# Optimization experiments

Measured on AMD Instinct MI355X. Metric: run time of the kernel, lower is better.

The kernel has to match this reference:

```python
import jax, jax.numpy as jnp
import numpy as np

EPS = 1e-07


def setup_inputs() -> dict:
    key = jax.random.key(0)
    ks = jax.random.split(key, 5)
    B, Cin, Cout, H, W, K, S = 8, 512, 512, 64, 64, 3, 512
    return {
        "x": jax.random.normal(ks[0], (B, Cin, H, W), dtype=jnp.float32),
        "style": jax.random.normal(ks[1], (B, S), dtype=jnp.float32),
        "weight": jax.random.normal(ks[2], (1, Cout, Cin, K, K), dtype=jnp.float32),
        "mod_w": jax.random.normal(ks[3], (Cin, S), dtype=jnp.float32) * (1.0 / np.sqrt(S)),
        "mod_b": jax.random.normal(ks[4], (Cin,), dtype=jnp.float32) * 0.01,
    }


def reference(x, style, weight, mod_w, mod_b):
    B, Cin, H, W = x.shape
    Cout, K = weight.shape[1], weight.shape[3]
    scale = 1.0 / np.sqrt(Cin * K * K)
    # modulation: plain linear (EqualLinear.forward never applies self.scale)
    s = (style @ mod_w.T + mod_b).reshape(B, 1, Cin, 1, 1)
    w = scale * weight * s  # [B, Cout, Cin, K, K]
    demod = jax.lax.rsqrt(jnp.sum(w * w, axis=(2, 3, 4), keepdims=True) + EPS)
    # NOTE: source divides by rsqrt (i.e. multiplies by sqrt) -- kept faithful
    w = w / demod
    w = w.reshape(B * Cout, Cin, K, K)
    xr = x.reshape(1, B * Cin, H, W)
    pad = (K - 1) // 2
    out = jax.lax.conv_general_dilated(
        xr, w,
        window_strides=(1, 1),
        padding=((pad, pad), (pad, pad)),
        dimension_numbers=("NCHW", "OIHW", "NCHW"),
        feature_group_count=B,
    )
    return out.reshape(B, Cout, H, W)
```

## Files before the change

kernel.cpp:

```cpp
#include <hip/hip_runtime.h>
#include <hip/hip_bf16.h>
#include <stdint.h>
#include <math.h>

#define EPSV 1e-7f
#define B_   8
#define CIN  512
#define COUT 512
#define HH   64
#define WW   64
#define SS   512
#define HP   66
#define WP   66
#define NP   (HH*WW)

typedef __attribute__((ext_vector_type(8))) short bf16x8;
typedef __attribute__((ext_vector_type(4))) float f32x4;

__global__ __launch_bounds__(256) void k_style(const float* __restrict__ style,
                                               const float* __restrict__ mod_w,
                                               const float* __restrict__ mod_b,
                                               float* __restrict__ s_out) {
    int tid = threadIdx.x;
    int id = blockIdx.x * 64 + (tid >> 2);
    int b = id >> 9, ci = id & 511, q = tid & 3;
    const float4* st = (const float4*)(style + (size_t)b * SS);
    const float4* mw = (const float4*)(mod_w + (size_t)ci * SS);
    float acc = 0.f;
    #pragma unroll
    for (int j = 0; j < 32; ++j) {
        float4 s4 = st[q * 32 + j];
        float4 w4 = mw[q * 32 + j];
        acc += s4.x * w4.x + s4.y * w4.y + s4.z * w4.z + s4.w * w4.w;
    }
    acc += __shfl_xor(acc, 1);
    acc += __shfl_xor(acc, 2);
    if (q == 0) s_out[id] = acc + mod_b[ci];
}

__global__ __launch_bounds__(256) void k_wmod(const float* __restrict__ weight,
                                              const float* __restrict__ s_in,
                                              __hip_bfloat16* __restrict__ wmod) {
    const int co  = blockIdx.x;
    const int tid = threadIdx.x;
    const int lane = tid & 63, wid = tid >> 6;
    const float scale = 0.014731391274719739f;
    float wv0[9], wv1[9];
    float wsq0 = 0.f, wsq1 = 0.f;
    {
        const float* wp0 = weight + ((size_t)co * CIN + tid) * 9;
        const float* wp1 = weight + ((size_t)co * CIN + tid + 256) * 9;
        #pragma unroll
        for (int t = 0; t < 9; ++t) { wv0[t] = wp0[t]; wsq0 += wv0[t] * wv0[t]; }
        #pragma unroll
        for (int t = 0; t < 9; ++t) { wv1[t] = wp1[t]; wsq1 += wv1[t] * wv1[t]; }
    }
    float sv0[8], sv1[8], sqb[8];
    #pragma unroll
    for (int b = 0; b < 8; ++b) {
        sv0[b] = s_in[b * CIN + tid] * scale;
        sv1[b] = s_in[b * CIN + tid + 256] * scale;
        sqb[b] = sv0[b] * sv0[b] * wsq0 + sv1[b] * sv1[b] * wsq1;
    }
    #pragma unroll
    for (int b = 0; b < 8; ++b) {
        float v = sqb[b];
        #pragma unroll
        for (int off = 32; off > 0; off >>= 1) v += __shfl_xor(v, off);
        sqb[b] = v;
    }
    __shared__ float red[4][8];
    if (lane == 0) {
        #pragma unroll
        for (int b = 0; b < 8; ++b) red[wid][b] = sqb[b];
    }
    __syncthreads();
    float dfac[8];
    #pragma unroll
    for (int b = 0; b < 8; ++b)
        dfac[b] = sqrtf(red[0][b] + red[1][b] + red[2][b] + red[3][b] + EPSV);
    #pragma unroll
    for (int b = 0; b < 8; ++b) {
        #pragma unroll
        for (int t = 0; t < 9; ++t) {
            size_t rowbase = ((size_t)((b * 9 + t) * COUT) + co) * CIN;
            wmod[rowbase + tid]       = __float2bfloat16(wv0[t] * sv0[b] * dfac[b]);
            wmod[rowbase + tid + 256] = __float2bfloat16(wv1[t] * sv1[b] * dfac[b]);
        }
    }
}

__global__ __launch_bounds__(256) void k_xpad(const float* __restrict__ x,
                                              __hip_bfloat16* __restrict__ xpad) {
    const int b = blockIdx.x >> 6;
    const int h = blockIdx.x & 63;
    const int tid = threadIdx.x;
    __shared__ float tile[64][65];
    for (int ci0 = 0; ci0 < CIN; ci0 += 64) {
        #pragma unroll
        for (int it = 0; it < 4; ++it) {
            int idx = it * 256 + tid;
            int w4 = idx & 15, cil = idx >> 4;
            float4 v = *(const float4*)&x[(((size_t)b * CIN + ci0 + cil) * HH + h) * WW + 4 * w4];
            tile[cil][4 * w4 + 0] = v.x; tile[cil][4 * w4 + 1] = v.y;
            tile[cil][4 * w4 + 2] = v.z; tile[cil][4 * w4 + 3] = v.w;
        }
        __syncthreads();
        #pragma unroll
        for (int it = 0; it < 4; ++it) {
            int idx = it * 256 + tid;
            int c4 = idx & 15, w = idx >> 4;
            __hip_bfloat16 t0 = __float2bfloat16(tile[4 * c4 + 0][w]);
            __hip_bfloat16 t1 = __float2bfloat16(tile[4 * c4 + 1][w]);
            __hip_bfloat16 t2 = __float2bfloat16(tile[4 * c4 + 2][w]);
            __hip_bfloat16 t3 = __float2bfloat16(tile[4 * c4 + 3][w]);
            ushort4 pk = make_ushort4(*(unsigned short*)&t0, *(unsigned short*)&t1,
                                      *(unsigned short*)&t2, *(unsigned short*)&t3);
            *(ushort4*)&xpad[(((size_t)b * HP + h + 1) * WP + (w + 1)) * CIN + ci0 + 4 * c4] = pk;
        }
        __syncthreads();
    }
    const size_t base = (size_t)b * HP * WP * CIN;
    const ushort4 z4 = make_ushort4(0, 0, 0, 0);
    {
        int wp = (tid < 128) ? 0 : 65;
        int e  = (tid & 127) * 4;
        *(ushort4*)&xpad[base + ((size_t)(h + 1) * WP + wp) * CIN + e] = z4;
    }
    if (h == 0 || h == 63) {
        int hp = (h == 0) ? 0 : 65;
        for (int i = tid; i < (HP * CIN) / 4; i += 256)
            *(ushort4*)&xpad[base + (size_t)hp * WP * CIN + (size_t)i * 4] = z4;
    }
}


#define MM(A,B,C) __builtin_amdgcn_mfma_f32_16x16x32_bf16(A,B,C,0,0,0)

#define GLDS(GP, LOFF) __builtin_amdgcn_global_load_lds( \
    (const __attribute__((address_space(1))) void*)(GP), \
    (__attribute__((address_space(3))) void*)(smem + (LOFF)), 16, 0, 0)

#define LDA(SB, M) (*(const bf16x8*)(aLds + ((SB)*16384 + (M)*1024)))
#define LDB(SB, N) (*(const bf16x8*)(bLds + ((SB)*16384 + (N)*1024)))

#define STAGE_A(KT, SB) { const int t3_ = (KT) >> 4, ci3_ = ((KT) & 15) * 32;   \
    const size_t aB_ = (size_t)(bb * 9 + t3_) * (COUT * CIN) + ci3_;            \
    GLDS(wmod + aB_ + gA0, (SB) * 16384 + ldsd);                                \
    GLDS(wmod + aB_ + gA1, (SB) * 16384 + 8192 + ldsd); }

#define STAGE_B(KT, SB) { const int t3_ = (KT) >> 4, ci3_ = ((KT) & 15) * 32;   \
    const int bO_ = ((t3_ / 3) * WP + (t3_ % 3)) * CIN + ci3_;                  \
    GLDS(xpad + bO_ + gB0, 65536 + (SB) * 16384 + ldsd);                        \
    GLDS(xpad + bO_ + gB1, 65536 + (SB) * 16384 + 8192 + ldsd); }

#define BARRIER asm volatile("s_barrier" ::: "memory")
#define VM8 asm volatile("s_waitcnt vmcnt(8)" ::: "memory");
#define VM4 asm volatile("s_waitcnt vmcnt(4)" ::: "memory");
#define VM0 asm volatile("s_waitcnt vmcnt(0)" ::: "memory");
#define VMNONE

#define CCOL(N, BV) acc[0][N]=MM(ca0,BV,acc[0][N]); acc[1][N]=MM(ca1,BV,acc[1][N]); \
                    acc[2][N]=MM(ca2,BV,acc[2][N]); acc[3][N]=MM(ca3,BV,acc[3][N]);
#define XCOL(N, BV) acc[4][N]=MM(x4_,BV,acc[4][N]); acc[5][N]=MM(x5_,BV,acc[5][N]); \
                    acc[6][N]=MM(x6_,BV,acc[6][N]); acc[7][N]=MM(x7_,BV,acc[7][N]);

#define KTILE3(KK, SB, DOSTAGE, WAITER, DONEXT) {                               \
    cb2 = LDB(SB, 2); cb3 = LDB(SB, 3);                                         \
    bf16x8 x4_ = LDA(SB,4), x5_ = LDA(SB,5), x6_ = LDA(SB,6), x7_ = LDA(SB,7);  \
    if (DOSTAGE) { STAGE_A((KK)+3, ((SB)+3)&3); STAGE_B((KK)+3, ((SB)+3)&3); }  \
    __builtin_amdgcn_s_setprio(1);                                              \
    CCOL(0, cb0) CCOL(1, cb1) CCOL(2, cb2) CCOL(3, cb3)                         \
    __builtin_amdgcn_s_setprio(0);                                              \
    __builtin_amdgcn_sched_barrier(0);                                          \
    WAITER                                                                      \
    BARRIER;                                                                    \
    __builtin_amdgcn_sched_barrier(0);                                          \
    if (DONEXT) { const int nsb_ = ((SB)+1)&3;                                  \
        ca0 = LDA(nsb_,0); ca1 = LDA(nsb_,1);                                   \
        ca2 = LDA(nsb_,2); ca3 = LDA(nsb_,3);                                   \
        nb0_ = LDB(nsb_,0); nb1_ = LDB(nsb_,1);                                 \
    }                                                                           \
    __builtin_amdgcn_s_setprio(1);                                              \
    XCOL(0, cb0) XCOL(1, cb1) XCOL(2, cb2) XCOL(3, cb3)                         \
    __builtin_amdgcn_s_setprio(0);                                              \
    cb0 = nb0_; cb1 = nb1_;                                                     \
}

__global__ __launch_bounds__(512, 2) void k_conv(const __hip_bfloat16* __restrict__ wmod,
                                                 const __hip_bfloat16* __restrict__ xpad,
                                                 float* __restrict__ out) {
    __shared__ __align__(16) char smem[131072];

    const int tid  = threadIdx.x;
    const int lane = tid & 63;
    const int wid  = tid >> 6;
    const int wr   = wid >> 2;
    const int wc   = wid & 3;
    const int frow = lane & 15;
    const int fk   = lane >> 4;

    const int bid = blockIdx.x;
    const int bb  = bid & 7;
    const int pt  = (bid >> 3) & 15;
    const int ct  = bid >> 7;
    const int co0 = ct * 256;
    const int p0  = pt * 256;

    const int xr = (fk ^ ((frow >> 1) & 3)) * 16;
    const char* aLds = smem + (wr * 8192 + frow * 64 + xr);
    const char* bLds = smem + 65536 + (wc * 4096 + frow * 64 + xr);

    const int ldsd = wid * 1024 + lane * 16;
    const int srow = wid * 16 + (lane >> 2);
    const int cg   = ((lane & 3) ^ ((lane >> 3) & 3)) * 8;
    const int gA0  = (co0 + srow) * CIN + cg;
    const int gA1  = (co0 + 128 + srow) * CIN + cg;
    const int pp0  = p0 + srow;
    const int pp1  = p0 + 128 + srow;
    const int gB0  = ((bb * HP + (pp0 >> 6)) * WP + (pp0 & 63)) * CIN + cg;
    const int gB1  = ((bb * HP + (pp1 >> 6)) * WP + (pp1 & 63)) * CIN + cg;

    f32x4 acc[8][4];
    #pragma unroll
    for (int m = 0; m < 8; ++m)
        #pragma unroll
        for (int n = 0; n < 4; ++n)
            acc[m][n] = (f32x4){0.f, 0.f, 0.f, 0.f};

    bf16x8 ca0, ca1, ca2, ca3, cb0, cb1, cb2, cb3, nb0_, nb1_;

    STAGE_A(0, 0) STAGE_B(0, 0)
    STAGE_A(1, 1) STAGE_B(1, 1)
    STAGE_A(2, 2) STAGE_B(2, 2)
    VM8;
    BARRIER;
    ca0 = LDA(0, 0); ca1 = LDA(0, 1); ca2 = LDA(0, 2); ca3 = LDA(0, 3);
    cb0 = LDB(0, 0); cb1 = LDB(0, 1);

    for (int k4 = 0; k4 < 140; k4 += 4) {
        KTILE3(k4 + 0, 0, 1, VM8, 1)
        KTILE3(k4 + 1, 1, 1, VM8, 1)
        KTILE3(k4 + 2, 2, 1, VM8, 1)
        KTILE3(k4 + 3, 3, 1, VM8, 1)
    }
    KTILE3(140, 0, 1, VM8, 1)
    KTILE3(141, 1, 0, VM4, 1)
    KTILE3(142, 2, 0, VM0, 1)
    KTILE3(143, 3, 0, VMNONE, 0)

    #pragma unroll
    for (int m = 0; m < 8; ++m) {
        int co = co0 + wr * 128 + m * 16 + fk * 4;
        #pragma unroll
        for (int n = 0; n < 4; ++n) {
            int p = p0 + wc * 64 + n * 16 + frow;
            #pragma unroll
            for (int j = 0; j < 4; ++j)
                out[((size_t)(bb * COUT + co + j)) * NP + p] = acc[m][n][j];
        }
    }
}

extern "C" void kernel_launch(void* const* d_in, const int* in_sizes, int n_in,
                              void* d_out, int out_size, void* d_ws, size_t ws_size,
                              hipStream_t stream) {
    const float* x      = (const float*)d_in[0];
    const float* style  = (const float*)d_in[1];
    const float* weight = (const float*)d_in[2];
    const float* mod_w  = (const float*)d_in[3];
    const float* mod_b  = (const float*)d_in[4];
    float* out = (float*)d_out;

    char* ws = (char*)d_ws;
    const size_t S_OFF    = 0;
    const size_t WMOD_OFF = 16384;
    const size_t XPAD_OFF = WMOD_OFF + (size_t)B_ * 9 * COUT * CIN * 2;

    float*          s_buf = (float*)(ws + S_OFF);
    __hip_bfloat16* wmod  = (__hip_bfloat16*)(ws + WMOD_OFF);
    __hip_bfloat16* xpad  = (__hip_bfloat16*)(ws + XPAD_OFF);

    k_style<<<64, 256, 0, stream>>>(style, mod_w, mod_b, s_buf);
    k_xpad<<<B_ * HH, 256, 0, stream>>>(x, xpad);
    k_wmod<<<512, 256, 0, stream>>>(weight, s_buf, wmod);

    k_conv<<<256, 512, 0, stream>>>(wmod, xpad, out);
}
```

Before: 160.5 us.

## Fold modulation into input and demod into epilogue; switch conv to 32x32 MFMA

The per-batch modulated weight tensor (8x9x512x512 bf16) is no longer built. The style scale is applied to the input during padding/bf16 conversion, and the demodulation factor is applied to the conv output in the epilogue. This shares one bf16 weight copy across batches and cuts weight-prep traffic. Separately, the conv inner loop moves from 16x16x32 to 32x32x16 bf16 MFMA with a new LDS read layout and fewer A/B fragment loads per tile. Rounding changes because the scale is now rounded into the bf16 input rather than the weights, and the new fragment indexing must match the existing swizzled LDS staging.

```diff
diff --git a/kernel.cpp b/kernel.cpp
--- a/kernel.cpp
+++ b/kernel.cpp
@@ -14,13 +14,16 @@
 #define WP   66
 #define NP   (HH*WW)
 
-typedef __attribute__((ext_vector_type(8))) short bf16x8;
-typedef __attribute__((ext_vector_type(4))) float f32x4;
-
-__global__ __launch_bounds__(256) void k_style(const float* __restrict__ style,
-                                               const float* __restrict__ mod_w,
-                                               const float* __restrict__ mod_b,
-                                               float* __restrict__ s_out) {
+typedef __attribute__((ext_vector_type(8)))  short bf16x8;
+typedef __attribute__((ext_vector_type(4)))  float f32x4;
+typedef __attribute__((ext_vector_type(16))) float f32x16;
+
+#define MODSCALE 0.014731391274719739f
+
+__global__ __launch_bounds__(256) void k_mod(const float* __restrict__ style,
+                                             const float* __restrict__ mod_w,
+                                             const float* __restrict__ mod_b,
+                                             float* __restrict__ m_out) {
     int tid = threadIdx.x;
     int id = blockIdx.x * 64 + (tid >> 2);
     int b = id >> 9, ci = id & 511, q = tid & 3;
@@ -35,62 +38,51 @@
     }
     acc += __shfl_xor(acc, 1);
     acc += __shfl_xor(acc, 2);
-    if (q == 0) s_out[id] = acc + mod_b[ci];
-}
-
-__global__ __launch_bounds__(256) void k_wmod(const float* __restrict__ weight,
-                                              const float* __restrict__ s_in,
-                                              __hip_bfloat16* __restrict__ wmod) {
-    const int co  = blockIdx.x;
+    if (q == 0) m_out[id] = MODSCALE * (acc + mod_b[ci]);
+}
+
+__global__ __launch_bounds__(256) void k_wprep(const float* __restrict__ weight,
+                                               __hip_bfloat16* __restrict__ wt,
+                                               float* __restrict__ wsq) {
+    const int co = blockIdx.x;
     const int tid = threadIdx.x;
-    const int lane = tid & 63, wid = tid >> 6;
-    const float scale = 0.014731391274719739f;
-    float wv0[9], wv1[9];
-    float wsq0 = 0.f, wsq1 = 0.f;
-    {
-        const float* wp0 = weight + ((size_t)co * CIN + tid) * 9;
-        const float* wp1 = weight + ((size_t)co * CIN + tid + 256) * 9;
-        #pragma unroll
-        for (int t = 0; t < 9; ++t) { wv0[t] = wp0[t]; wsq0 += wv0[t] * wv0[t]; }
-        #pragma unroll
-        for (int t = 0; t < 9; ++t) { wv1[t] = wp1[t]; wsq1 += wv1[t] * wv1[t]; }
-    }
-    float sv0[8], sv1[8], sqb[8];
-    #pragma unroll
-    for (int b = 0; b < 8; ++b) {
-        sv0[b] = s_in[b * CIN + tid] * scale;
-        sv1[b] = s_in[b * CIN + tid + 256] * scale;
-        sqb[b] = sv0[b] * sv0[b] * wsq0 + sv1[b] * sv1[b] * wsq1;
-    }
-    #pragma unroll
-    for (int b = 0; b < 8; ++b) {
-        float v = sqb[b];
-        #pragma unroll
-        for (int off = 32; off > 0; off >>= 1) v += __shfl_xor(v, off);
-        sqb[b] = v;
-    }
-    __shared__ float red[4][8];
-    if (lane == 0) {
-        #pragma unroll
-        for (int b = 0; b < 8; ++b) red[wid][b] = sqb[b];
-    }
-    __syncthreads();
-    float dfac[8];
-    #pragma unroll
-    for (int b = 0; b < 8; ++b)
-        dfac[b] = sqrtf(red[0][b] + red[1][b] + red[2][b] + red[3][b] + EPSV);
-    #pragma unroll
-    for (int b = 0; b < 8; ++b) {
-        #pragma unroll
-        for (int t = 0; t < 9; ++t) {
-            size_t rowbase = ((size_t)((b * 9 + t) * COUT) + co) * CIN;
-            wmod[rowbase + tid]       = __float2bfloat16(wv0[t] * sv0[b] * dfac[b]);
-            wmod[rowbase + tid + 256] = __float2bfloat16(wv1[t] * sv1[b] * dfac[b]);
-        }
-    }
+    #pragma unroll
+    for (int j = 0; j < 2; ++j) {
+        int ci = tid + j * 256;
+        const float* wp = weight + ((size_t)co * CIN + ci) * 9;
+        float w[9], sq = 0.f;
+        #pragma unroll
+        for (int t = 0; t < 9; ++t) { w[t] = wp[t]; sq += w[t] * w[t]; }
+        #pragma unroll
+        for (int t = 0; t < 9; ++t)
+            wt[(size_t)t * COUT * CIN + (size_t)co * CIN + ci] = __float2bfloat16(w[t]);
+        wsq[co * CIN + ci] = sq;
+    }
+}
+
+__global__ __launch_bounds__(256) void k_dfac(const float* __restrict__ wsq,
+                                              const float* __restrict__ m_buf,
+                                              float* __restrict__ dfac) {
+    int tid = threadIdx.x;
+    int id = blockIdx.x * 64 + (tid >> 2);
+    int b = id >> 9, co = id & 511, q = tid & 3;
+    const float4* wq = (const float4*)(wsq + (size_t)co * CIN);
+    const float4* mb = (const float4*)(m_buf + (size_t)b * CIN);
+    float acc = 0.f;
+    #pragma unroll
+    for (int j = 0; j < 32; ++j) {
+        float4 w4 = wq[q * 32 + j];
+        float4 m4 = mb[q * 32 + j];
+        acc += w4.x * m4.x * m4.x + w4.y * m4.y * m4.y
+             + w4.z * m4.z * m4.z + w4.w * m4.w * m4.w;
+    }
+    acc += __shfl_xor(acc, 1);
+    acc += __shfl_xor(acc, 2);
+    if (q == 0) dfac[id] = sqrtf(acc + EPSV);
 }
 
 __global__ __launch_bounds__(256) void k_xpad(const float* __restrict__ x,
+                                              const float* __restrict__ m_buf,
                                               __hip_bfloat16* __restrict__ xpad) {
     const int b = blockIdx.x >> 6;
     const int h = blockIdx.x & 63;
@@ -110,10 +102,11 @@
         for (int it = 0; it < 4; ++it) {
             int idx = it * 256 + tid;
             int c4 = idx & 15, w = idx >> 4;
-            __hip_bfloat16 t0 = __float2bfloat16(tile[4 * c4 + 0][w]);
-            __hip_bfloat16 t1 = __float2bfloat16(tile[4 * c4 + 1][w]);
-            __hip_bfloat16 t2 = __float2bfloat16(tile[4 * c4 + 2][w]);
-            __hip_bfloat16 t3 = __float2bfloat16(tile[4 * c4 + 3][w]);
+            float4 mv = *(const float4*)&m_buf[b * CIN + ci0 + 4 * c4];
+            __hip_bfloat16 t0 = __float2bfloat16(tile[4 * c4 + 0][w] * mv.x);
+            __hip_bfloat16 t1 = __float2bfloat16(tile[4 * c4 + 1][w] * mv.y);
+            __hip_bfloat16 t2 = __float2bfloat16(tile[4 * c4 + 2][w] * mv.z);
+            __hip_bfloat16 t3 = __float2bfloat16(tile[4 * c4 + 3][w] * mv.w);
             ushort4 pk = make_ushort4(*(unsigned short*)&t0, *(unsigned short*)&t1,
                                       *(unsigned short*)&t2, *(unsigned short*)&t3);
             *(ushort4*)&xpad[(((size_t)b * HP + h + 1) * WP + (w + 1)) * CIN + ci0 + 4 * c4] = pk;
@@ -135,19 +128,19 @@
 }
 
 
-#define MM(A,B,C) __builtin_amdgcn_mfma_f32_16x16x32_bf16(A,B,C,0,0,0)
+#define MM32(A,B,C) __builtin_amdgcn_mfma_f32_32x32x16_bf16(A,B,C,0,0,0)
 
 #define GLDS(GP, LOFF) __builtin_amdgcn_global_load_lds( \
     (const __attribute__((address_space(1))) void*)(GP), \
     (__attribute__((address_space(3))) void*)(smem + (LOFF)), 16, 0, 0)
 
-#define LDA(SB, M) (*(const bf16x8*)(aLds + ((SB)*16384 + (M)*1024)))
-#define LDB(SB, N) (*(const bf16x8*)(bLds + ((SB)*16384 + (N)*1024)))
+#define LDA32(SB, M, XR) (*(const bf16x8*)(aBase + ((SB)*16384 + (M)*2048 + (XR))))
+#define LDB32(SB, N, XR) (*(const bf16x8*)(bBase + ((SB)*16384 + (N)*2048 + (XR))))
 
 #define STAGE_A(KT, SB) { const int t3_ = (KT) >> 4, ci3_ = ((KT) & 15) * 32;   \
-    const size_t aB_ = (size_t)(bb * 9 + t3_) * (COUT * CIN) + ci3_;            \
-    GLDS(wmod + aB_ + gA0, (SB) * 16384 + ldsd);                                \
-    GLDS(wmod + aB_ + gA1, (SB) * 16384 + 8192 + ldsd); }
+    const size_t aB_ = (size_t)t3_ * (COUT * CIN) + ci3_;                       \
+    GLDS(wt + aB_ + gA0, (SB) * 16384 + ldsd);                                  \
+    GLDS(wt + aB_ + gA1, (SB) * 16384 + 8192 + ldsd); }
 
 #define STAGE_B(KT, SB) { const int t3_ = (KT) >> 4, ci3_ = ((KT) & 15) * 32;   \
     const int bO_ = ((t3_ / 3) * WP + (t3_ % 3)) * CIN + ci3_;                  \
@@ -160,35 +153,36 @@
 #define VM0 asm volatile("s_waitcnt vmcnt(0)" ::: "memory");
 #define VMNONE
 
-#define CCOL(N, BV) acc[0][N]=MM(ca0,BV,acc[0][N]); acc[1][N]=MM(ca1,BV,acc[1][N]); \
-                    acc[2][N]=MM(ca2,BV,acc[2][N]); acc[3][N]=MM(ca3,BV,acc[3][N]);
-#define XCOL(N, BV) acc[4][N]=MM(x4_,BV,acc[4][N]); acc[5][N]=MM(x5_,BV,acc[5][N]); \
-                    acc[6][N]=MM(x6_,BV,acc[6][N]); acc[7][N]=MM(x7_,BV,acc[7][N]);
-
-#define KTILE3(KK, SB, DOSTAGE, WAITER, DONEXT) {                               \
-    cb2 = LDB(SB, 2); cb3 = LDB(SB, 3);                                         \
-    bf16x8 x4_ = LDA(SB,4), x5_ = LDA(SB,5), x6_ = LDA(SB,6), x7_ = LDA(SB,7);  \
+#define CL(A0,A1,A2,A3,B0,B1) \
+    acc[0][0]=MM32(A0,B0,acc[0][0]); acc[1][0]=MM32(A1,B0,acc[1][0]); \
+    acc[2][0]=MM32(A2,B0,acc[2][0]); acc[3][0]=MM32(A3,B0,acc[3][0]); \
+    acc[0][1]=MM32(A0,B1,acc[0][1]); acc[1][1]=MM32(A1,B1,acc[1][1]); \
+    acc[2][1]=MM32(A2,B1,acc[2][1]); acc[3][1]=MM32(A3,B1,acc[3][1]);
+
+#define KTILE32(KK, SB, DOSTAGE, WAITER, DONEXT) {                              \
+    bf16x8 a10=LDA32(SB,0,xr1), a11=LDA32(SB,1,xr1),                            \
+           a12=LDA32(SB,2,xr1), a13=LDA32(SB,3,xr1);                            \
+    bf16x8 b10=LDB32(SB,0,xr1), b11=LDB32(SB,1,xr1);                            \
     if (DOSTAGE) { STAGE_A((KK)+3, ((SB)+3)&3); STAGE_B((KK)+3, ((SB)+3)&3); }  \
     __builtin_amdgcn_s_setprio(1);                                              \
-    CCOL(0, cb0) CCOL(1, cb1) CCOL(2, cb2) CCOL(3, cb3)                         \
+    CL(a00,a01,a02,a03,b00,b01)                                                 \
     __builtin_amdgcn_s_setprio(0);                                              \
     __builtin_amdgcn_sched_barrier(0);                                          \
     WAITER                                                                      \
     BARRIER;                                                                    \
     __builtin_amdgcn_sched_barrier(0);                                          \
     if (DONEXT) { const int nsb_ = ((SB)+1)&3;                                  \
-        ca0 = LDA(nsb_,0); ca1 = LDA(nsb_,1);                                   \
-        ca2 = LDA(nsb_,2); ca3 = LDA(nsb_,3);                                   \
-        nb0_ = LDB(nsb_,0); nb1_ = LDB(nsb_,1);                                 \
-    }                                                                           \
+        a00=LDA32(nsb_,0,xr0); a01=LDA32(nsb_,1,xr0);                           \
+        a02=LDA32(nsb_,2,xr0); a03=LDA32(nsb_,3,xr0);                           \
+        b00=LDB32(nsb_,0,xr0); b01=LDB32(nsb_,1,xr0); }                         \
     __builtin_amdgcn_s_setprio(1);                                              \
-    XCOL(0, cb0) XCOL(1, cb1) XCOL(2, cb2) XCOL(3, cb3)                         \
+    CL(a10,a11,a12,a13,b10,b11)                                                 \
     __builtin_amdgcn_s_setprio(0);                                              \
-    cb0 = nb0_; cb1 = nb1_;                                                     \
-}
-
-__global__ __launch_bounds__(512, 2) void k_conv(const __hip_bfloat16* __restrict__ wmod,
+}
+
+__global__ __launch_bounds__(512, 2) void k_conv(const __hip_bfloat16* __restrict__ wt,
                                                  const __hip_bfloat16* __restrict__ xpad,
+                                                 const float* __restrict__ dfac,
                                                  float* __restrict__ out) {
     __shared__ __align__(16) char smem[131072];
 
@@ -197,8 +191,8 @@
     const int wid  = tid >> 6;
     const int wr   = wid >> 2;
     const int wc   = wid & 3;
-    const int frow = lane & 15;
-    const int fk   = lane >> 4;
+    const int l31  = lane & 31;
+    const int hi   = lane >> 5;
 
     const int bid = blockIdx.x;
     const int bb  = bid & 7;
@@ -207,9 +201,11 @@
     const int co0 = ct * 256;
     const int p0  = pt * 256;
 
-    const int xr = (fk ^ ((frow >> 1) & 3)) * 16;
-    const char* aLds = smem + (wr * 8192 + frow * 64 + xr);
-    const char* bLds = smem + 65536 + (wc * 4096 + frow * 64 + xr);
+    const int swz = (l31 >> 1) & 3;
+    const int xr0 = ((0 + hi) ^ swz) * 16;
+    const int xr1 = ((2 + hi) ^ swz) * 16;
+    const char* aBase = smem + ((wr * 128 + l31) * 64);
+    const char* bBase = smem + 65536 + ((wc * 64 + l31) * 64);
 
     const int ldsd = wid * 1024 + lane * 16;
     const int srow = wid * 16 + (lane >> 2);
@@ -221,43 +217,46 @@
     const int gB0  = ((bb * HP + (pp0 >> 6)) * WP + (pp0 & 63)) * CIN + cg;
     const int gB1  = ((bb * HP + (pp1 >> 6)) * WP + (pp1 & 63)) * CIN + cg;
 
-    f32x4 acc[8][4];
-    #pragma unroll
-    for (int m = 0; m < 8; ++m)
-        #pragma unroll
-        for (int n = 0; n < 4; ++n)
-            acc[m][n] = (f32x4){0.f, 0.f, 0.f, 0.f};
-
-    bf16x8 ca0, ca1, ca2, ca3, cb0, cb1, cb2, cb3, nb0_, nb1_;
+    f32x16 acc[4][2];
+    #pragma unroll
+    for (int m = 0; m < 4; ++m)
+        #pragma unroll
+        for (int n = 0; n < 2; ++n)
+            acc[m][n] = (f32x16)(0.f);
+
+    bf16x8 a00, a01, a02, a03, b00, b01;
 
     STAGE_A(0, 0) STAGE_B(0, 0)
     STAGE_A(1, 1) STAGE_B(1, 1)
     STAGE_A(2, 2) STAGE_B(2, 2)
     VM8;
     BARRIER;
-    ca0 = LDA(0, 0); ca1 = LDA(0, 1); ca2 = LDA(0, 2); ca3 = LDA(0, 3);
-    cb0 = LDB(0, 0); cb1 = LDB(0, 1);
+    a00 = LDA32(0,0,xr0); a01 = LDA32(0,1,xr0); a02 = LDA32(0,2,xr0); a03 = LDA32(0,3,xr0);
+    b00 = LDB32(0,0,xr0); b01 = LDB32(0,1,xr0);
 
     for (int k4 = 0; k4 < 140; k4 += 4) {
-        KTILE3(k4 + 0, 0, 1, VM8, 1)
-        KTILE3(k4 + 1, 1, 1, VM8, 1)
-        KTILE3(k4 + 2, 2, 1, VM8, 1)
-        KTILE3(k4 + 3, 3, 1, VM8, 1)
-    }
-    KTILE3(140, 0, 1, VM8, 1)
-    KTILE3(141, 1, 0, VM4, 1)
-    KTILE3(142, 2, 0, VM0, 1)
-    KTILE3(143, 3, 0, VMNONE, 0)
-
-    #pragma unroll
-    for (int m = 0; m < 8; ++m) {
-        int co = co0 + wr * 128 + m * 16 + fk * 4;
-        #pragma unroll
-        for (int n = 0; n < 4; ++n) {
-            int p = p0 + wc * 64 + n * 16 + frow;
+        KTILE32(k4 + 0, 0, 1, VM8, 1)
+        KTILE32(k4 + 1, 1, 1, VM8, 1)
+        KTILE32(k4 + 2, 2, 1, VM8, 1)
+        KTILE32(k4 + 3, 3, 1, VM8, 1)
+    }
+    KTILE32(140, 0, 1, VM8, 1)
+    KTILE32(141, 1, 0, VM4, 1)
+    KTILE32(142, 2, 0, VM0, 1)
+    KTILE32(143, 3, 0, VMNONE, 0)
+
+    const float* dfb = dfac + bb * COUT + co0 + wr * 128;
+    #pragma unroll
+    for (int m = 0; m < 4; ++m) {
+        #pragma unroll
+        for (int n = 0; n < 2; ++n) {
+            int p = p0 + wc * 64 + n * 32 + l31;
             #pragma unroll
-            for (int j = 0; j < 4; ++j)
-                out[((size_t)(bb * COUT + co + j)) * NP + p] = acc[m][n][j];
+            for (int r = 0; r < 16; ++r) {
+                int row = m * 32 + (r & 3) + 8 * (r >> 2) + 4 * hi;
+                out[((size_t)(bb * COUT + co0 + wr * 128 + row)) * NP + p] =
+                    acc[m][n][r] * dfb[row];
+            }
         }
     }
 }
@@ -273,17 +272,22 @@
     float* out = (float*)d_out;
 
     char* ws = (char*)d_ws;
-    const size_t S_OFF    = 0;
-    const size_t WMOD_OFF = 16384;
-    const size_t XPAD_OFF = WMOD_OFF + (size_t)B_ * 9 * COUT * CIN * 2;
-
-    float*          s_buf = (float*)(ws + S_OFF);
-    __hip_bfloat16* wmod  = (__hip_bfloat16*)(ws + WMOD_OFF);
+    const size_t M_OFF    = 0;
+    const size_t WSQ_OFF  = 16384;
+    const size_t DFAC_OFF = WSQ_OFF + (size_t)COUT * CIN * 4;
+    const size_t WT_OFF   = DFAC_OFF + 16384;
+    const size_t XPAD_OFF = WT_OFF + (size_t)9 * COUT * CIN * 2;
+
+    float*          m_buf = (float*)(ws + M_OFF);
+    float*          wsq   = (float*)(ws + WSQ_OFF);
+    float*          dfac  = (float*)(ws + DFAC_OFF);
+    __hip_bfloat16* wt    = (__hip_bfloat16*)(ws + WT_OFF);
     __hip_bfloat16* xpad  = (__hip_bfloat16*)(ws + XPAD_OFF);
 
-    k_style<<<64, 256, 0, stream>>>(style, mod_w, mod_b, s_buf);
-    k_xpad<<<B_ * HH, 256, 0, stream>>>(x, xpad);
-    k_wmod<<<512, 256, 0, stream>>>(weight, s_buf, wmod);
-
-    k_conv<<<256, 512, 0, stream>>>(wmod, xpad, out);
-}
+    k_mod<<<64, 256, 0, stream>>>(style, mod_w, mod_b, m_buf);
+    k_wprep<<<512, 256, 0, stream>>>(weight, wt, wsq);
+    k_xpad<<<B_ * HH, 256, 0, stream>>>(x, m_buf, xpad);
+    k_dfac<<<64, 256, 0, stream>>>(wsq, m_buf, dfac);
+
+    k_conv<<<256, 512, 0, stream>>>(wt, xpad, dfac, out);
+}
```

New measurement: 181.4 us. +13.1%, slower.

## Fold style modulation into input and demodulation into output epilogue

Applied to the files above, without the earlier changes.

Moves the per-batch style scale off the weights and onto the input channels during the padding/bf16 conversion. The demodulation factor is now applied per output channel in the conv epilogue, so only one shared bf16 weight tensor is built instead of eight per-batch copies. This removes most of the weight-prep write traffic and lets conv A-tiles be shared across batches through L2. It also coalesces the weight read through shared memory. Rounding order changes slightly, since the input is scaled before bf16 conversion.

```diff
diff --git a/kernel.cpp b/kernel.cpp
--- a/kernel.cpp
+++ b/kernel.cpp
@@ -14,13 +14,15 @@
 #define WP   66
 #define NP   (HH*WW)
 
-typedef __attribute__((ext_vector_type(8))) short bf16x8;
-typedef __attribute__((ext_vector_type(4))) float f32x4;
-
-__global__ __launch_bounds__(256) void k_style(const float* __restrict__ style,
-                                               const float* __restrict__ mod_w,
-                                               const float* __restrict__ mod_b,
-                                               float* __restrict__ s_out) {
+typedef __attribute__((ext_vector_type(8)))  short bf16x8;
+typedef __attribute__((ext_vector_type(4)))  float f32x4;
+
+#define MODSCALE 0.014731391274719739f
+
+__global__ __launch_bounds__(256) void k_mod(const float* __restrict__ style,
+                                             const float* __restrict__ mod_w,
+                                             const float* __restrict__ mod_b,
+                                             float* __restrict__ m_out) {
     int tid = threadIdx.x;
     int id = blockIdx.x * 64 + (tid >> 2);
     int b = id >> 9, ci = id & 511, q = tid & 3;
@@ -35,62 +37,63 @@
     }
     acc += __shfl_xor(acc, 1);
     acc += __shfl_xor(acc, 2);
-    if (q == 0) s_out[id] = acc + mod_b[ci];
-}
-
-__global__ __launch_bounds__(256) void k_wmod(const float* __restrict__ weight,
-                                              const float* __restrict__ s_in,
-                                              __hip_bfloat16* __restrict__ wmod) {
+    if (q == 0) m_out[id] = MODSCALE * (acc + mod_b[ci]);
+}
+
+__global__ __launch_bounds__(256) void k_wprep(const float* __restrict__ weight,
+                                               const float* __restrict__ m_buf,
+                                               __hip_bfloat16* __restrict__ wt,
+                                               float* __restrict__ dfac) {
     const int co  = blockIdx.x;
     const int tid = threadIdx.x;
     const int lane = tid & 63, wid = tid >> 6;
-    const float scale = 0.014731391274719739f;
-    float wv0[9], wv1[9];
-    float wsq0 = 0.f, wsq1 = 0.f;
-    {
-        const float* wp0 = weight + ((size_t)co * CIN + tid) * 9;
-        const float* wp1 = weight + ((size_t)co * CIN + tid + 256) * 9;
-        #pragma unroll
-        for (int t = 0; t < 9; ++t) { wv0[t] = wp0[t]; wsq0 += wv0[t] * wv0[t]; }
-        #pragma unroll
-        for (int t = 0; t < 9; ++t) { wv1[t] = wp1[t]; wsq1 += wv1[t] * wv1[t]; }
-    }
-    float sv0[8], sv1[8], sqb[8];
+    __shared__ float wrow[4608];
+    __shared__ float red[4][8];
+    const float2* wsrc = (const float2*)(weight + (size_t)co * 4608);
+    #pragma unroll
+    for (int i = 0; i < 9; ++i)
+        *(float2*)&wrow[(i * 256 + tid) * 2] = wsrc[i * 256 + tid];
+    __syncthreads();
+    float w0[9], w1[9], sq0 = 0.f, sq1 = 0.f;
+    #pragma unroll
+    for (int t = 0; t < 9; ++t) {
+        w0[t] = wrow[tid * 9 + t];
+        w1[t] = wrow[(tid + 256) * 9 + t];
+        sq0 += w0[t] * w0[t];
+        sq1 += w1[t] * w1[t];
+    }
+    float part[8];
     #pragma unroll
     for (int b = 0; b < 8; ++b) {
-        sv0[b] = s_in[b * CIN + tid] * scale;
-        sv1[b] = s_in[b * CIN + tid + 256] * scale;
-        sqb[b] = sv0[b] * sv0[b] * wsq0 + sv1[b] * sv1[b] * wsq1;
+        float m0 = m_buf[b * CIN + tid];
+        float m1 = m_buf[b * CIN + tid + 256];
+        part[b] = sq0 * m0 * m0 + sq1 * m1 * m1;
     }
     #pragma unroll
     for (int b = 0; b < 8; ++b) {
-        float v = sqb[b];
+        float v = part[b];
         #pragma unroll
         for (int off = 32; off > 0; off >>= 1) v += __shfl_xor(v, off);
-        sqb[b] = v;
-    }
-    __shared__ float red[4][8];
+        part[b] = v;
+    }
     if (lane == 0) {
         #pragma unroll
-        for (int b = 0; b < 8; ++b) red[wid][b] = sqb[b];
+        for (int b = 0; b < 8; ++b) red[wid][b] = part[b];
+    }
+    #pragma unroll
+    for (int t = 0; t < 9; ++t) {
+        size_t base = (size_t)t * COUT * CIN + (size_t)co * CIN;
+        wt[base + tid]       = __float2bfloat16(w0[t]);
+        wt[base + tid + 256] = __float2bfloat16(w1[t]);
     }
     __syncthreads();
-    float dfac[8];
-    #pragma unroll
-    for (int b = 0; b < 8; ++b)
-        dfac[b] = sqrtf(red[0][b] + red[1][b] + red[2][b] + red[3][b] + EPSV);
-    #pragma unroll
-    for (int b = 0; b < 8; ++b) {
-        #pragma unroll
-        for (int t = 0; t < 9; ++t) {
-            size_t rowbase = ((size_t)((b * 9 + t) * COUT) + co) * CIN;
-            wmod[rowbase + tid]       = __float2bfloat16(wv0[t] * sv0[b] * dfac[b]);
-            wmod[rowbase + tid + 256] = __float2bfloat16(wv1[t] * sv1[b] * dfac[b]);
-        }
-    }
+    if (tid < 8)
+        dfac[tid * COUT + co] =
+            sqrtf(red[0][tid] + red[1][tid] + red[2][tid] + red[3][tid] + EPSV);
 }
 
 __global__ __launch_bounds__(256) void k_xpad(const float* __restrict__ x,
+                                              const float* __restrict__ m_buf,
                                               __hip_bfloat16* __restrict__ xpad) {
     const int b = blockIdx.x >> 6;
     const int h = blockIdx.x & 63;
@@ -110,10 +113,11 @@
         for (int it = 0; it < 4; ++it) {
             int idx = it * 256 + tid;
             int c4 = idx & 15, w = idx >> 4;
-            __hip_bfloat16 t0 = __float2bfloat16(tile[4 * c4 + 0][w]);
-            __hip_bfloat16 t1 = __float2bfloat16(tile[4 * c4 + 1][w]);
-            __hip_bfloat16 t2 = __float2bfloat16(tile[4 * c4 + 2][w]);
-            __hip_bfloat16 t3 = __float2bfloat16(tile[4 * c4 + 3][w]);
+            float4 mv = *(const float4*)&m_buf[b * CIN + ci0 + 4 * c4];
+            __hip_bfloat16 t0 = __float2bfloat16(tile[4 * c4 + 0][w] * mv.x);
+            __hip_bfloat16 t1 = __float2bfloat16(tile[4 * c4 + 1][w] * mv.y);
+            __hip_bfloat16 t2 = __float2bfloat16(tile[4 * c4 + 2][w] * mv.z);
+            __hip_bfloat16 t3 = __float2bfloat16(tile[4 * c4 + 3][w] * mv.w);
             ushort4 pk = make_ushort4(*(unsigned short*)&t0, *(unsigned short*)&t1,
                                       *(unsigned short*)&t2, *(unsigned short*)&t3);
             *(ushort4*)&xpad[(((size_t)b * HP + h + 1) * WP + (w + 1)) * CIN + ci0 + 4 * c4] = pk;
@@ -145,9 +149,9 @@
 #define LDB(SB, N) (*(const bf16x8*)(bLds + ((SB)*16384 + (N)*1024)))
 
 #define STAGE_A(KT, SB) { const int t3_ = (KT) >> 4, ci3_ = ((KT) & 15) * 32;   \
-    const size_t aB_ = (size_t)(bb * 9 + t3_) * (COUT * CIN) + ci3_;            \
-    GLDS(wmod + aB_ + gA0, (SB) * 16384 + ldsd);                                \
-    GLDS(wmod + aB_ + gA1, (SB) * 16384 + 8192 + ldsd); }
+    const size_t aB_ = (size_t)t3_ * (COUT * CIN) + ci3_;                       \
+    GLDS(wt + aB_ + gA0, (SB) * 16384 + ldsd);                                  \
+    GLDS(wt + aB_ + gA1, (SB) * 16384 + 8192 + ldsd); }
 
 #define STAGE_B(KT, SB) { const int t3_ = (KT) >> 4, ci3_ = ((KT) & 15) * 32;   \
     const int bO_ = ((t3_ / 3) * WP + (t3_ % 3)) * CIN + ci3_;                  \
@@ -187,8 +191,9 @@
     cb0 = nb0_; cb1 = nb1_;                                                     \
 }
 
-__global__ __launch_bounds__(512, 2) void k_conv(const __hip_bfloat16* __restrict__ wmod,
+__global__ __launch_bounds__(512, 2) void k_conv(const __hip_bfloat16* __restrict__ wt,
                                                  const __hip_bfloat16* __restrict__ xpad,
+                                                 const float* __restrict__ dfac,
                                                  float* __restrict__ out) {
     __shared__ __align__(16) char smem[131072];
 
@@ -249,15 +254,19 @@
     KTILE3(142, 2, 0, VM0, 1)
     KTILE3(143, 3, 0, VMNONE, 0)
 
+    const float* dfb = dfac + bb * COUT;
     #pragma unroll
     for (int m = 0; m < 8; ++m) {
         int co = co0 + wr * 128 + m * 16 + fk * 4;
+        float d0 = dfb[co + 0], d1 = dfb[co + 1], d2 = dfb[co + 2], d3 = dfb[co + 3];
         #pragma unroll
         for (int n = 0; n < 4; ++n) {
             int p = p0 + wc * 64 + n * 16 + frow;
-            #pragma unroll
-            for (int j = 0; j < 4; ++j)
-                out[((size_t)(bb * COUT + co + j)) * NP + p] = acc[m][n][j];
+            size_t ob = ((size_t)(bb * COUT + co)) * NP + p;
+            out[ob]          = acc[m][n][0] * d0;
+            out[ob + NP]     = acc[m][n][1] * d1;
+            out[ob + 2 * NP] = acc[m][n][2] * d2;
+            out[ob + 3 * NP] = acc[m][n][3] * d3;
         }
     }
 }
@@ -273,17 +282,19 @@
     float* out = (float*)d_out;
 
     char* ws = (char*)d_ws;
-    const size_t S_OFF    = 0;
-    const size_t WMOD_OFF = 16384;
-    const size_t XPAD_OFF = WMOD_OFF + (size_t)B_ * 9 * COUT * CIN * 2;
-
-    float*          s_buf = (float*)(ws + S_OFF);
-    __hip_bfloat16* wmod  = (__hip_bfloat16*)(ws + WMOD_OFF);
+    const size_t M_OFF    = 0;
+    const size_t DFAC_OFF = 16384;
+    const size_t WT_OFF   = 32768;
+    const size_t XPAD_OFF = WT_OFF + (size_t)9 * COUT * CIN * 2;
+
+    float*          m_buf = (float*)(ws + M_OFF);
+    float*          dfac  = (float*)(ws + DFAC_OFF);
+    __hip_bfloat16* wt    = (__hip_bfloat16*)(ws + WT_OFF);
     __hip_bfloat16* xpad  = (__hip_bfloat16*)(ws + XPAD_OFF);
 
-    k_style<<<64, 256, 0, stream>>>(style, mod_w, mod_b, s_buf);
-    k_xpad<<<B_ * HH, 256, 0, stream>>>(x, xpad);
-    k_wmod<<<512, 256, 0, stream>>>(weight, s_buf, wmod);
-
-    k_conv<<<256, 512, 0, stream>>>(wmod, xpad, out);
-}
+    k_mod<<<64, 256, 0, stream>>>(style, mod_w, mod_b, m_buf);
+    k_wprep<<<512, 256, 0, stream>>>(weight, m_buf, wt, dfac);
+    k_xpad<<<B_ * HH, 256, 0, stream>>>(x, m_buf, xpad);
+
+    k_conv<<<256, 512, 0, stream>>>(wt, xpad, dfac, out);
+}
```

Result: no change. 158.2 us (-1.4%).
